# Optimization experiments

Hardware: AMD Instinct MI355X
Metric: run time of the kernel (lower is better)

## Reference

```python
import jax, jax.numpy as jnp
import numpy as np

B, C, H, W = 4, 256, 64, 64
G = 32          # GroupNorm groups
KH = KW = 3     # deformable kernel
K = KH * KW
EPS = 1e-5
PAD = 1
DIL = 1
STRIDE = 1


def conv3x3(x, w, b):
    # plain 3x3 conv, stride 1, pad 1 (offset-prediction conv)
    y = jax.lax.conv_general_dilated(
        x, w, window_strides=(1, 1), padding=((1, 1), (1, 1)),
        dimension_numbers=('NCHW', 'OIHW', 'NCHW'))
    return y + b[None, :, None, None]


def group_norm(x, gamma, beta):
    b, c, h, w = x.shape
    xr = x.reshape(b, G, -1)
    mu = jnp.mean(xr, axis=-1, keepdims=True)
    var = jnp.var(xr, axis=-1, keepdims=True)
    xn = ((xr - mu) * jax.lax.rsqrt(var + EPS)).reshape(b, c, h, w)
    return xn * gamma[None, :, None, None] + beta[None, :, None, None]


def deform_conv(x, offset, weight):
    # x: [B,Cin,H,W]; offset: [B,2*K,H,W] as (dy,dx) pairs per kernel tap;
    # weight: [Cout,Cin,KH,KW]. DeformConv v1, no bias, stride=1, pad=1.
    b, cin, h, w = x.shape
    cout = weight.shape[0]
    off = offset.reshape(b, K, 2, h, w)
    dy, dx = off[:, :, 0], off[:, :, 1]          # [B,K,H,W]

    ky = (jnp.arange(K) // KW).astype(x.dtype)   # kernel tap row
    kx = (jnp.arange(K) % KW).astype(x.dtype)    # kernel tap col
    hh = jnp.arange(h, dtype=x.dtype)
    ww = jnp.arange(w, dtype=x.dtype)

    # fractional sampling coordinates, shape [B,K,H,W]
    py = dy + hh[None, None, :, None] * STRIDE - PAD + ky[None, :, None, None] * DIL
    px = dx + ww[None, None, None, :] * STRIDE - PAD + kx[None, :, None, None] * DIL

    y0 = jnp.floor(py)
    x0 = jnp.floor(px)
    ly = py - y0   # bilinear fractions
    lx = px - x0

    xf = x.reshape(b, cin, h * w)

    def gather(yi, xi):
        valid = ((yi >= 0) & (yi < h) & (xi >= 0) & (xi < w)).astype(x.dtype)
        yc = jnp.clip(yi, 0, h - 1).astype(jnp.int32)
        xc = jnp.clip(xi, 0, w - 1).astype(jnp.int32)
        idx = (yc * w + xc).reshape(b, 1, K * h * w)
        g = jnp.take_along_axis(xf, idx, axis=2).reshape(b, cin, K, h, w)
        return g * valid[:, None]

    # accumulate 4 bilinear corners -> sampled patches [B,Cin,K,H,W]
    val = gather(y0, x0) * ((1 - ly) * (1 - lx))[:, None]
    val = val + gather(y0, x0 + 1) * ((1 - ly) * lx)[:, None]
    val = val + gather(y0 + 1, x0) * (ly * (1 - lx))[:, None]
    val = val + gather(y0 + 1, x0 + 1) * (ly * lx)[:, None]

    wk = weight.reshape(cout, cin, K)
    return jnp.einsum('bckhw,ock->bohw', val, wk)


def setup_inputs() -> dict:
    key = jax.random.key(0)
    ks = jax.random.split(key, 12)
    fan = 1.0 / np.sqrt(C * K)
    off_scale = 0.01  # small offsets -> near-grid sampling, as after training-time zero-init
    return {
        'x':      jax.random.normal(ks[0], (B, C, H, W), jnp.float32),
        'w_off1': jax.random.normal(ks[1], (2 * K, C, KH, KW), jnp.float32) * off_scale,
        'b_off1': jnp.zeros((2 * K,), jnp.float32),
        'w_off2': jax.random.normal(ks[2], (2 * K, C, KH, KW), jnp.float32) * off_scale,
        'b_off2': jnp.zeros((2 * K,), jnp.float32),
        'w_def1': jax.random.normal(ks[3], (C, C, KH, KW), jnp.float32) * fan,
        'w_def2': jax.random.normal(ks[4], (C, C, KH, KW), jnp.float32) * fan,
        'gamma1': jnp.ones((C,), jnp.float32),
        'beta1':  jnp.zeros((C,), jnp.float32),
        'gamma2': jnp.ones((C,), jnp.float32),
        'beta2':  jnp.zeros((C,), jnp.float32),
    }


def reference(x, w_off1, b_off1, w_off2, b_off2, w_def1, w_def2,
              gamma1, beta1, gamma2, beta2):
    residual = x
    offset = conv3x3(x, w_off1, b_off1)
    out = deform_conv(x, offset, w_def1)
    out = jax.nn.relu(group_norm(out, gamma1, beta1))
    offset2 = conv3x3(out, w_off2, b_off2)
    out = deform_conv(out, offset2, w_def2)
    out = group_norm(out, gamma2, beta2)
    out = jax.nn.relu(out + residual)
    return out
```

## Files before the change

kernel.cpp:

```cpp
#include <hip/hip_runtime.h>
#include <hip/hip_bf16.h>

typedef unsigned int uint;
typedef unsigned short ushort;
typedef __attribute__((ext_vector_type(8))) short bfrag_t;
typedef __attribute__((ext_vector_type(4))) short s4_t;
typedef __attribute__((ext_vector_type(4))) float f4_t;
typedef __attribute__((ext_vector_type(2))) float f2_t;

#define EPSV 1e-5f

__device__ __forceinline__ float4 ld4(const float* p) { return *(const float4*)p; }
__device__ __forceinline__ void st4(float* p, float4 v) { *(float4*)p = v; }

__device__ __forceinline__ ushort f2bf(float f) {
    union { float f; uint u; } v; v.f = f;
    uint r = v.u + 0x7fffu + ((v.u >> 16) & 1u);
    return (ushort)(r >> 16);
}
__device__ __forceinline__ float bf2f(ushort s) {
    union { uint u; float f; } v; v.u = ((uint)s) << 16;
    return v.f;
}
__device__ __forceinline__ float bfhi(uint u) { union { uint u; float f; } v; v.u = u & 0xffff0000u; return v.f; }
__device__ __forceinline__ float bflo(uint u) { union { uint u; float f; } v; v.u = u << 16; return v.f; }
__device__ __forceinline__ uint pk2(float a, float b) { return (uint)f2bf(a) | ((uint)f2bf(b) << 16); }
__device__ __forceinline__ uint pkrn(float a, float b) {
    union { __hip_bfloat162 h; uint u; } v;
    v.h = __float22bfloat162_rn(make_float2(a, b));
    return v.u;
}

__global__ __launch_bounds__(256) void prep_all(const float* __restrict__ wd1, const float* __restrict__ wd2,
                                                const float* __restrict__ wo1, const float* __restrict__ wo2,
                                                const float* __restrict__ x,
                                                ushort* __restrict__ oT1, ushort* __restrict__ oT2,
                                                ushort* __restrict__ oO1, ushort* __restrict__ oO2,
                                                ushort* __restrict__ xb, float* __restrict__ gnacc) {
    __shared__ float lds[64][65];
    int bid = blockIdx.x;
    int tid = threadIdx.x;
    if (bid < 512) {
        int co = bid & 255;
        int sel = bid >> 8;
        const float* w = sel ? wd2 : wd1;
        ushort* o = sel ? oT2 : oT1;
        const float* p = w + (co * 256 + tid) * 9;
        float v[9];
#pragma unroll
        for (int k = 0; k < 9; ++k) v[k] = p[k];
#pragma unroll
        for (int k = 0; k < 9; ++k) o[(k * 256 + co) * 256 + tid] = f2bf(v[k]);
    } else if (bid < 576) {
        int idx = bid - 512;
        int co = idx & 31;
        int sel = idx >> 5;
        const float* w = sel ? wo2 : wo1;
        ushort* o = sel ? oO2 : oO1;
        float v[9] = {0.f,0.f,0.f,0.f,0.f,0.f,0.f,0.f,0.f};
        if (co < 18) {
            const float* p = w + (co * 256 + tid) * 9;
#pragma unroll
            for (int k = 0; k < 9; ++k) v[k] = p[k];
        }
#pragma unroll
        for (int k = 0; k < 9; ++k) o[(k * 32 + co) * 256 + tid] = f2bf(v[k]);
        if (idx == 0) { gnacc[tid] = 0.f; gnacc[256 + tid] = 0.f; }
    } else {
        int b2 = bid - 576;
        int cb = b2 & 3, y = (b2 >> 2) & 63, b = b2 >> 8;
        int c0 = cb << 6;
#pragma unroll
        for (int i = 0; i < 4; ++i) {
            int q = tid + (i << 8);
            int c_l = q >> 4, x4 = (q & 15) << 2;
            float4 v = ld4(&x[((b * 256 + c0 + c_l) << 12) + (y << 6) + x4]);
            lds[c_l][x4 + 0] = v.x; lds[c_l][x4 + 1] = v.y; lds[c_l][x4 + 2] = v.z; lds[c_l][x4 + 3] = v.w;
        }
        __syncthreads();
#pragma unroll
        for (int i = 0; i < 4; ++i) {
            int q = tid + (i << 8);
            int x_l = q >> 4, c4 = (q & 15) << 2;
            s4_t v;
            v.x = (short)f2bf(lds[c4 + 0][x_l]); v.y = (short)f2bf(lds[c4 + 1][x_l]);
            v.z = (short)f2bf(lds[c4 + 2][x_l]); v.w = (short)f2bf(lds[c4 + 3][x_l]);
            *(s4_t*)&xb[(((b << 12) + (y << 6) + x_l) << 8) + c0 + c4] = v;
        }
    }
}

__global__ __launch_bounds__(256, 4) void offconv4(const ushort* __restrict__ xb, const ushort* __restrict__ wO,
                                                   const float* __restrict__ bias, float* __restrict__ offb) {
    __shared__ float red2[4][64][9];
    int bidx = blockIdx.x;
    int tile = (bidx & 7) * 128 + (bidx >> 3);
    int px0 = tile << 4;
    int tid = threadIdx.x;
    int wave = tid >> 6, lane = tid & 63;
    int lr = lane & 15, lq = lane >> 4;
    int pxl = px0 + lr;
    int b = pxl >> 12, y = (pxl >> 6) & 63, x = pxl & 63;
    int cibase = wave << 6;

    f4_t acc0 = (f4_t){0.f,0.f,0.f,0.f}, acc1 = (f4_t){0.f,0.f,0.f,0.f};
#pragma unroll
    for (int tap = 0; tap < 9; ++tap) {
        int ky = tap / 3, kx = tap - ky * 3;
        int yy = y + ky - 1, xx = x + kx - 1;
        bool valid = (yy >= 0) && (yy < 64) && (xx >= 0) && (xx < 64);
        const ushort* arow = xb + ((((b << 6) + yy) << 6) + xx) * 256 + cibase;
        const ushort* wrow = wO + ((tap << 5) << 8) + cibase;
#pragma unroll
        for (int s = 0; s < 2; ++s) {
            int cio = (s << 5) + (lq << 3);
            bfrag_t afr = (bfrag_t){0,0,0,0,0,0,0,0};
            if (valid) afr = *(const bfrag_t*)(arow + cio);
            bfrag_t b0 = *(const bfrag_t*)(wrow + (lr << 8) + cio);
            bfrag_t b1 = *(const bfrag_t*)(wrow + ((16 + lr) << 8) + cio);
            acc0 = __builtin_amdgcn_mfma_f32_16x16x32_bf16(afr, b0, acc0, 0, 0, 0);
            acc1 = __builtin_amdgcn_mfma_f32_16x16x32_bf16(afr, b1, acc1, 0, 0, 0);
        }
    }
#pragma unroll
    for (int r = 0; r < 4; ++r) {
        red2[wave][lane][r] = acc0[r];
        red2[wave][lane][4 + r] = acc1[r];
    }
    __syncthreads();
    if (tid < 64) {
        float v[8];
#pragma unroll
        for (int e = 0; e < 8; ++e)
            v[e] = red2[0][tid][e] + red2[1][tid][e] + red2[2][tid][e] + red2[3][tid][e];
        int lr2 = tid & 15, lq2 = tid >> 4;
        float bv0 = bias[lr2];
        float bv1 = (lr2 < 2) ? bias[16 + lr2] : 0.f;
#pragma unroll
        for (int e = 0; e < 4; ++e) {
            int row = (px0 + (lq2 << 2) + e) * 18;
            offb[row + lr2] = v[e] + bv0;
            if (lr2 < 2) offb[row + 16 + lr2] = v[4 + e] + bv1;
        }
    }
}

__global__ __launch_bounds__(512, 2) void deform_mfma(const ushort* __restrict__ xb, const float* __restrict__ offb,
                                                      const ushort* __restrict__ wT, ushort* __restrict__ outb,
                                                      float* __restrict__ gnacc) {
    __shared__ short As[2][16384];
    __shared__ float red[64];

    int bidx = blockIdx.x;
    int tile = (bidx & 7) * 32 + (bidx >> 3);
    int px0 = tile << 6;
    int bb = px0 >> 12;

    int tid = threadIdx.x;
    int wave = tid >> 6;
    int lane = tid & 63;
    int lr = lane & 15, lq = lane >> 4;

    if (tid < 64) red[tid] = 0.f;

    int gpx = tid >> 3;
    int gl = tid & 7;
    int pxg = px0 + gpx;
    int gy = (pxg >> 6) & 63, gx = pxg & 63;
    int gbase = (pxg >> 12) << 12;
    const float* offp = offb + pxg * 18;

    f4_t acc[4][2];
#pragma unroll
    for (int m = 0; m < 4; ++m)
#pragma unroll
        for (int n = 0; n < 2; ++n) acc[m][n] = (f4_t){0.f,0.f,0.f,0.f};

    uint4 q[4][4];
    float cw0, cw1, cw2, cw3;

    auto gload = [&](int tap) {
        int ky = tap / 3, kx = tap - ky * 3;
        float2 of = *(const float2*)(offp + 2 * tap);
        float py  = of.x + (float)(gy - 1 + ky);
        float pxx = of.y + (float)(gx - 1 + kx);
        float y0f = floorf(py), x0f = floorf(pxx);
        float ly = py - y0f, lx = pxx - x0f;
        int y0 = (int)y0f, x0 = (int)x0f;
        int y1 = y0 + 1, x1 = x0 + 1;
        float wy0 = ((uint)y0 < 64u) ? (1.f - ly) : 0.f;
        float wy1 = ((uint)y1 < 64u) ? ly : 0.f;
        float wx0 = ((uint)x0 < 64u) ? (1.f - lx) : 0.f;
        float wx1 = ((uint)x1 < 64u) ? lx : 0.f;
        int y0c = min(max(y0, 0), 63), y1c = min(max(y1, 0), 63);
        int x0c = min(max(x0, 0), 63), x1c = min(max(x1, 0), 63);
        cw0 = wy0 * wx0; cw1 = wy0 * wx1; cw2 = wy1 * wx0; cw3 = wy1 * wx1;
        const ushort* s0 = xb + ((gbase + (y0c << 6) + x0c) << 8) + (gl << 3);
        const ushort* s1 = xb + ((gbase + (y0c << 6) + x1c) << 8) + (gl << 3);
        const ushort* s2 = xb + ((gbase + (y1c << 6) + x0c) << 8) + (gl << 3);
        const ushort* s3 = xb + ((gbase + (y1c << 6) + x1c) << 8) + (gl << 3);
#pragma unroll
        for (int u = 0; u < 4; ++u) {
            q[0][u] = *(const uint4*)(s0 + (u << 6));
            q[1][u] = *(const uint4*)(s1 + (u << 6));
            q[2][u] = *(const uint4*)(s2 + (u << 6));
            q[3][u] = *(const uint4*)(s3 + (u << 6));
        }
    };

    auto gstore = [&](int buf) {
        f2_t w0 = {cw0, cw0}, w1 = {cw1, cw1}, w2 = {cw2, cw2}, w3 = {cw3, cw3};
#pragma unroll
        for (int u = 0; u < 4; ++u) {
            uint4 q0 = q[0][u], q1 = q[1][u], q2 = q[2][u], q3 = q[3][u];
            f2_t a0 = w0 * (f2_t){bflo(q0.x), bfhi(q0.x)} + w1 * (f2_t){bflo(q1.x), bfhi(q1.x)}
                    + w2 * (f2_t){bflo(q2.x), bfhi(q2.x)} + w3 * (f2_t){bflo(q3.x), bfhi(q3.x)};
            f2_t a1 = w0 * (f2_t){bflo(q0.y), bfhi(q0.y)} + w1 * (f2_t){bflo(q1.y), bfhi(q1.y)}
                    + w2 * (f2_t){bflo(q2.y), bfhi(q2.y)} + w3 * (f2_t){bflo(q3.y), bfhi(q3.y)};
            f2_t a2 = w0 * (f2_t){bflo(q0.z), bfhi(q0.z)} + w1 * (f2_t){bflo(q1.z), bfhi(q1.z)}
                    + w2 * (f2_t){bflo(q2.z), bfhi(q2.z)} + w3 * (f2_t){bflo(q3.z), bfhi(q3.z)};
            f2_t a3 = w0 * (f2_t){bflo(q0.w), bfhi(q0.w)} + w1 * (f2_t){bflo(q1.w), bfhi(q1.w)}
                    + w2 * (f2_t){bflo(q2.w), bfhi(q2.w)} + w3 * (f2_t){bflo(q3.w), bfhi(q3.w)};
            uint4 o;
            o.x = pkrn(a0.x, a0.y); o.y = pkrn(a1.x, a1.y);
            o.z = pkrn(a2.x, a2.y); o.w = pkrn(a3.x, a3.y);
            int kblk = (u << 3) + gl;
            int chunk = (kblk << 6) + (gpx ^ (kblk & 7));
            *(uint4*)&As[buf][chunk << 3] = o;
        }
    };

    auto gemm = [&](int tap, int buf) {
        const ushort* wbase = wT + ((tap << 8) + (wave << 5) + lr) * 256 + (lq << 3);
        bfrag_t bf0[8], bf1[8];
#pragma unroll
        for (int s = 0; s < 8; ++s) {
            bf0[s] = *(const bfrag_t*)(wbase + (s << 5));
            bf1[s] = *(const bfrag_t*)(wbase + (16 << 8) + (s << 5));
        }
#pragma unroll
        for (int s = 0; s < 8; ++s) {
            int kblk = (s << 2) + lq;
            int kx7 = kblk & 7;
#pragma unroll
            for (int m = 0; m < 4; ++m) {
                int chunk = (kblk << 6) + (((m << 4) + lr) ^ kx7);
                bfrag_t a = *(const bfrag_t*)&As[buf][chunk << 3];
                acc[m][0] = __builtin_amdgcn_mfma_f32_16x16x32_bf16(a, bf0[s], acc[m][0], 0, 0, 0);
                acc[m][1] = __builtin_amdgcn_mfma_f32_16x16x32_bf16(a, bf1[s], acc[m][1], 0, 0, 0);
            }
        }
    };

    gload(0);
    gstore(0);
    __syncthreads();
    for (int tap = 0; tap < 9; ++tap) {
        if (tap < 8) gload(tap + 1);
        gemm(tap, tap & 1);
        if (tap < 8) gstore((tap + 1) & 1);
        __syncthreads();
    }

    int cob = wave << 5;
#pragma unroll
    for (int n = 0; n < 2; ++n) {
        int co = cob + (n << 4) + lr;
        float s = 0.f, s2 = 0.f;
#pragma unroll
        for (int m = 0; m < 4; ++m)
#pragma unroll
            for (int r = 0; r < 4; ++r) {
                float v = acc[m][n][r];
                s += v; s2 += v * v;
                As[0][(((m << 4) + (lq << 2) + r) << 8) + co] = (short)f2bf(v);
            }
        int g = co >> 3;
        atomicAdd(&red[g], s);
        atomicAdd(&red[32 + g], s2);
    }
    __syncthreads();
    {
        const uint4* src = (const uint4*)&As[0][0];
        uint4* dst = (uint4*)&outb[px0 << 8];
#pragma unroll
        for (int i = 0; i < 4; ++i)
            dst[tid + (i << 9)] = src[tid + (i << 9)];
    }
    if (tid < 32) {
        atomicAdd(&gnacc[((bb << 5) + tid) * 2], red[tid]);
        atomicAdd(&gnacc[((bb << 5) + tid) * 2 + 1], red[32 + tid]);
    }
}

__global__ __launch_bounds__(256) void gn_apply_relu_bb(const ushort* __restrict__ in, const float* __restrict__ gnacc,
                                                        const float* __restrict__ gamma, const float* __restrict__ beta,
                                                        ushort* __restrict__ outb) {
    int q = blockIdx.x * 256 + threadIdx.x;
    int e0 = q << 3;
    int c0 = e0 & 255;
    int b = e0 >> 20;
    int g = c0 >> 3;
    float2 a = *(const float2*)(gnacc + ((b << 5) + g) * 2);
    float mean = a.x * (1.f / 32768.f);
    float var = fmaxf(a.y * (1.f / 32768.f) - mean * mean, 0.f);
    float rstd = rsqrtf(var + EPSV);
    uint4 v = *(const uint4*)(in + e0);
    float4 ga0 = ld4(&gamma[c0]), ga1 = ld4(&gamma[c0 + 4]);
    float4 be0 = ld4(&beta[c0]),  be1 = ld4(&beta[c0 + 4]);
    uint4 o;
    o.x = pk2(fmaxf((bflo(v.x) - mean) * rstd * ga0.x + be0.x, 0.f),
              fmaxf((bfhi(v.x) - mean) * rstd * ga0.y + be0.y, 0.f));
    o.y = pk2(fmaxf((bflo(v.y) - mean) * rstd * ga0.z + be0.z, 0.f),
              fmaxf((bfhi(v.y) - mean) * rstd * ga0.w + be0.w, 0.f));
    o.z = pk2(fmaxf((bflo(v.z) - mean) * rstd * ga1.x + be1.x, 0.f),
              fmaxf((bfhi(v.z) - mean) * rstd * ga1.y + be1.y, 0.f));
    o.w = pk2(fmaxf((bflo(v.w) - mean) * rstd * ga1.z + be1.z, 0.f),
              fmaxf((bfhi(v.w) - mean) * rstd * ga1.w + be1.w, 0.f));
    *(uint4*)&outb[e0] = o;
}

__global__ __launch_bounds__(256) void final_bf16(const ushort* __restrict__ v2, const float* __restrict__ gnacc,
                                                  const float* __restrict__ gamma, const float* __restrict__ beta,
                                                  const float* __restrict__ xin, float* __restrict__ out) {
    __shared__ float lds[64][65];
    int bid = blockIdx.x;
    int cb = bid & 3, y = (bid >> 2) & 63, b = bid >> 8;
    int c0 = cb << 6;
    int tid = threadIdx.x;
#pragma unroll
    for (int i = 0; i < 4; ++i) {
        int q = tid + (i << 8);
        int x_l = q >> 4, c4 = (q & 15) << 2;
        s4_t v = *(const s4_t*)&v2[(((b << 12) + (y << 6) + x_l) << 8) + c0 + c4];
        lds[c4 + 0][x_l] = bf2f((ushort)v.x); lds[c4 + 1][x_l] = bf2f((ushort)v.y);
        lds[c4 + 2][x_l] = bf2f((ushort)v.z); lds[c4 + 3][x_l] = bf2f((ushort)v.w);
    }
    __syncthreads();
#pragma unroll
    for (int i = 0; i < 4; ++i) {
        int q = tid + (i << 8);
        int c_l = q >> 4, x4 = (q & 15) << 2;
        int c = c0 + c_l;
        int g = c >> 3;
        float2 a = *(const float2*)(gnacc + ((b << 5) + g) * 2);
        float mean = a.x * (1.f / 32768.f);
        float var = fmaxf(a.y * (1.f / 32768.f) - mean * mean, 0.f);
        float rstd = rsqrtf(var + EPSV);
        float ga = gamma[c], be = beta[c];
        const float* xp = &xin[((b << 8) + c) * 4096 + (y << 6) + x4];
        float4 r = ld4(xp);
        float4 o;
        o.x = fmaxf((lds[c_l][x4 + 0] - mean) * rstd * ga + be + r.x, 0.f);
        o.y = fmaxf((lds[c_l][x4 + 1] - mean) * rstd * ga + be + r.y, 0.f);
        o.z = fmaxf((lds[c_l][x4 + 2] - mean) * rstd * ga + be + r.z, 0.f);
        o.w = fmaxf((lds[c_l][x4 + 3] - mean) * rstd * ga + be + r.w, 0.f);
        st4(&out[((b << 8) + c) * 4096 + (y << 6) + x4], o);
    }
}

extern "C" void kernel_launch(void* const* d_in, const int* in_sizes, int n_in,
                              void* d_out, int out_size, void* d_ws, size_t ws_size,
                              hipStream_t stream) {
    (void)in_sizes; (void)n_in; (void)out_size; (void)ws_size;
    const float* x      = (const float*)d_in[0];
    const float* w_off1 = (const float*)d_in[1];
    const float* b_off1 = (const float*)d_in[2];
    const float* w_off2 = (const float*)d_in[3];
    const float* b_off2 = (const float*)d_in[4];
    const float* w_def1 = (const float*)d_in[5];
    const float* w_def2 = (const float*)d_in[6];
    const float* gamma1 = (const float*)d_in[7];
    const float* beta1  = (const float*)d_in[8];
    const float* gamma2 = (const float*)d_in[9];
    const float* beta2  = (const float*)d_in[10];
    float* out = (float*)d_out;

    float* ws = (float*)d_ws;
    float*  xb_f   = ws;
    float*  xb2_f  = xb_f + 2097152;
    float*  wT1_f  = xb2_f + 2097152;
    float*  wT2_f  = wT1_f + 294912;
    float*  wO1_f  = wT2_f + 294912;
    float*  wO2_f  = wO1_f + 36864;
    float*  offb   = wO2_f + 36864;
    float*  gnacc1 = offb + 294912;
    float*  gnacc2 = gnacc1 + 256;

    ushort* xb  = (ushort*)xb_f;
    ushort* v2b = (ushort*)xb_f;
    ushort* xb2 = (ushort*)xb2_f;
    ushort* wT1 = (ushort*)wT1_f;
    ushort* wT2 = (ushort*)wT2_f;
    ushort* wO1 = (ushort*)wO1_f;
    ushort* wO2 = (ushort*)wO2_f;
    ushort* t1b = (ushort*)d_out;

    prep_all<<<1600, 256, 0, stream>>>(w_def1, w_def2, w_off1, w_off2, x,
                                       wT1, wT2, wO1, wO2, xb, gnacc1);
    offconv4<<<1024, 256, 0, stream>>>(xb, wO1, b_off1, offb);
    deform_mfma<<<256, 512, 0, stream>>>(xb, offb, wT1, t1b, gnacc1);
    gn_apply_relu_bb<<<2048, 256, 0, stream>>>(t1b, gnacc1, gamma1, beta1, xb2);
    offconv4<<<1024, 256, 0, stream>>>(xb2, wO2, b_off2, offb);
    deform_mfma<<<256, 512, 0, stream>>>(xb2, offb, wT2, v2b, gnacc2);
    final_bf16<<<1024, 256, 0, stream>>>(v2b, gnacc2, gamma2, beta2, x, out);
}
```

Before: 262.7 us.

## Retile offset conv to full-row blocks with 8-wave channel split

The offset-prediction conv now processes a full 64-pixel image row per 512-thread block, with 8 waves each owning 32 input channels. Each wave reuses one set of weight fragments across four 16-pixel M-tiles. Whole rows that fall out of bounds are skipped per tap. This cuts redundant weight loads and block count, at the cost of a larger LDS reduction buffer and fewer blocks, which means less parallelism across the device.

```diff
diff --git a/kernel.cpp b/kernel.cpp
--- a/kernel.cpp
+++ b/kernel.cpp
@@ -90,58 +90,63 @@
     }
 }
 
-__global__ __launch_bounds__(256, 4) void offconv4(const ushort* __restrict__ xb, const ushort* __restrict__ wO,
+__global__ __launch_bounds__(512, 2) void offconv8(const ushort* __restrict__ xb, const ushort* __restrict__ wO,
                                                    const float* __restrict__ bias, float* __restrict__ offb) {
-    __shared__ float red2[4][64][9];
+    __shared__ float red2[8][64][33];
     int bidx = blockIdx.x;
-    int tile = (bidx & 7) * 128 + (bidx >> 3);
-    int px0 = tile << 4;
+    int tile = (bidx & 7) * 32 + (bidx >> 3);
+    int px0 = tile << 6;
+    int b = tile >> 6;
+    int y = tile & 63;
     int tid = threadIdx.x;
     int wave = tid >> 6, lane = tid & 63;
     int lr = lane & 15, lq = lane >> 4;
-    int pxl = px0 + lr;
-    int b = pxl >> 12, y = (pxl >> 6) & 63, x = pxl & 63;
-    int cibase = wave << 6;
-
-    f4_t acc0 = (f4_t){0.f,0.f,0.f,0.f}, acc1 = (f4_t){0.f,0.f,0.f,0.f};
+    int cio = (wave << 5) + (lq << 3);
+
+    f4_t acc[4][2];
+#pragma unroll
+    for (int m = 0; m < 4; ++m)
+#pragma unroll
+        for (int n = 0; n < 2; ++n) acc[m][n] = (f4_t){0.f,0.f,0.f,0.f};
+
 #pragma unroll
     for (int tap = 0; tap < 9; ++tap) {
         int ky = tap / 3, kx = tap - ky * 3;
-        int yy = y + ky - 1, xx = x + kx - 1;
-        bool valid = (yy >= 0) && (yy < 64) && (xx >= 0) && (xx < 64);
-        const ushort* arow = xb + ((((b << 6) + yy) << 6) + xx) * 256 + cibase;
-        const ushort* wrow = wO + ((tap << 5) << 8) + cibase;
-#pragma unroll
-        for (int s = 0; s < 2; ++s) {
-            int cio = (s << 5) + (lq << 3);
-            bfrag_t afr = (bfrag_t){0,0,0,0,0,0,0,0};
-            if (valid) afr = *(const bfrag_t*)(arow + cio);
-            bfrag_t b0 = *(const bfrag_t*)(wrow + (lr << 8) + cio);
-            bfrag_t b1 = *(const bfrag_t*)(wrow + ((16 + lr) << 8) + cio);
-            acc0 = __builtin_amdgcn_mfma_f32_16x16x32_bf16(afr, b0, acc0, 0, 0, 0);
-            acc1 = __builtin_amdgcn_mfma_f32_16x16x32_bf16(afr, b1, acc1, 0, 0, 0);
-        }
-    }
-#pragma unroll
-    for (int r = 0; r < 4; ++r) {
-        red2[wave][lane][r] = acc0[r];
-        red2[wave][lane][4 + r] = acc1[r];
-    }
+        int yy = y + ky - 1;
+        if ((uint)yy < 64u) {
+            const ushort* wrow = wO + ((tap << 5) << 8) + cio;
+            bfrag_t b0 = *(const bfrag_t*)(wrow + (lr << 8));
+            bfrag_t b1 = *(const bfrag_t*)(wrow + ((16 + lr) << 8));
+            const ushort* arow = xb + (((b << 6) + yy) << 14) + cio;
+#pragma unroll
+            for (int m = 0; m < 4; ++m) {
+                int xx = (m << 4) + lr + kx - 1;
+                bfrag_t afr = (bfrag_t){0,0,0,0,0,0,0,0};
+                if ((uint)xx < 64u) afr = *(const bfrag_t*)(arow + (xx << 8));
+                acc[m][0] = __builtin_amdgcn_mfma_f32_16x16x32_bf16(afr, b0, acc[m][0], 0, 0, 0);
+                acc[m][1] = __builtin_amdgcn_mfma_f32_16x16x32_bf16(afr, b1, acc[m][1], 0, 0, 0);
+            }
+        }
+    }
+#pragma unroll
+    for (int m = 0; m < 4; ++m)
+#pragma unroll
+        for (int n = 0; n < 2; ++n)
+#pragma unroll
+            for (int r = 0; r < 4; ++r)
+                red2[wave][lane][(m << 3) + (n << 2) + r] = acc[m][n][r];
     __syncthreads();
-    if (tid < 64) {
-        float v[8];
-#pragma unroll
-        for (int e = 0; e < 8; ++e)
-            v[e] = red2[0][tid][e] + red2[1][tid][e] + red2[2][tid][e] + red2[3][tid][e];
-        int lr2 = tid & 15, lq2 = tid >> 4;
-        float bv0 = bias[lr2];
-        float bv1 = (lr2 < 2) ? bias[16 + lr2] : 0.f;
-#pragma unroll
-        for (int e = 0; e < 4; ++e) {
-            int row = (px0 + (lq2 << 2) + e) * 18;
-            offb[row + lr2] = v[e] + bv0;
-            if (lr2 < 2) offb[row + 16 + lr2] = v[4 + e] + bv1;
-        }
+#pragma unroll
+    for (int e = 0; e < 4; ++e) {
+        int oi = tid + (e << 9);
+        int px = oi >> 5, co = oi & 31;
+        int m = px >> 4, w4 = px & 15;
+        int lanes = ((w4 >> 2) << 4) + (co & 15);
+        int elem = (m << 3) + ((co >> 4) << 2) + (w4 & 3);
+        float v = 0.f;
+#pragma unroll
+        for (int w = 0; w < 8; ++w) v += red2[w][lanes][elem];
+        if (co < 18) offb[(px0 + px) * 18 + co] = v + bias[co];
     }
 }
 
@@ -398,10 +403,10 @@
 
     prep_all<<<1600, 256, 0, stream>>>(w_def1, w_def2, w_off1, w_off2, x,
                                        wT1, wT2, wO1, wO2, xb, gnacc1);
-    offconv4<<<1024, 256, 0, stream>>>(xb, wO1, b_off1, offb);
+    offconv8<<<256, 512, 0, stream>>>(xb, wO1, b_off1, offb);
     deform_mfma<<<256, 512, 0, stream>>>(xb, offb, wT1, t1b, gnacc1);
     gn_apply_relu_bb<<<2048, 256, 0, stream>>>(t1b, gnacc1, gamma1, beta1, xb2);
-    offconv4<<<1024, 256, 0, stream>>>(xb2, wO2, b_off2, offb);
+    offconv8<<<256, 512, 0, stream>>>(xb2, wO2, b_off2, offb);
     deform_mfma<<<256, 512, 0, stream>>>(xb2, offb, wT2, v2b, gnacc2);
     final_bf16<<<1024, 256, 0, stream>>>(v2b, gnacc2, gamma2, beta2, x, out);
 }
```

Result: faster. 239.1 us (-9.0%).
